# Kernel tuning notes

Hardware: AMD Instinct MI355X
Metric: run time of the kernel (lower is better)

Reference implementation:

```python
import jax, jax.numpy as jnp
import numpy as np

TEMPERATURE = 0.01
VMIN, VMAX = -1.0, 1.0
NUM_VALUES = 256


def setup_inputs() -> dict:
    key = jax.random.key(0)
    k_img, k_cmap = jax.random.split(key)
    image = jax.random.uniform(k_img, (4, 3, 512, 512), dtype=jnp.float32)
    cmap = jax.random.uniform(k_cmap, (NUM_VALUES, 3), dtype=jnp.float32)
    idx = jnp.arange(NUM_VALUES, dtype=jnp.float32)
    v_i = VMIN + (VMAX - VMIN) * idx / (NUM_VALUES - 1)
    return {"image": image, "cmap": cmap, "v_i": v_i}


def reference(image, cmap, v_i):
    # image: (N, 3, H, W) -> (N, H, W, 3)
    img = jnp.transpose(image, (0, 2, 3, 1))
    # squared euclidean distance to each of the 256 colormap colors
    # dist[n,h,w,k] = sum_c (img[n,h,w,c] - cmap[k,c])^2
    diff = img[..., None, :] - cmap  # (N, H, W, K, 3)
    distances = jnp.sum(diff * diff, axis=-1)  # (N, H, W, K)
    weights = jax.nn.softmax(-distances / TEMPERATURE, axis=-1)
    velocities = jnp.einsum('nhwk,k->nhw', weights, v_i)
    return velocities
```

## Files before the change

### kernel.cpp

```cpp
#include <hip/hip_runtime.h>


typedef float v2f __attribute__((ext_vector_type(2)));

#define HWSZ 262144
#define NPIX 1048576
#define K2F  144.2695040888963f

__global__ __launch_bounds__(256) void rgb2vel_prep(
    const float* __restrict__ cmap, const float* __restrict__ v_i,
    float4* __restrict__ ab, float* __restrict__ vv) {
  int k = threadIdx.x;
  float cx = cmap[k * 3 + 0];
  float cy = cmap[k * 3 + 1];
  float cz = cmap[k * 3 + 2];
  float4 r;
  r.x = 2.0f * K2F * cx;
  r.y = 2.0f * K2F * cy;
  r.z = 2.0f * K2F * cz;
  r.w = -K2F * (cx * cx + cy * cy + cz * cz);
  ab[k] = r;
  vv[k] = v_i[k];
}

__global__ __launch_bounds__(256) void rgb2vel_main(
    const float* __restrict__ img, const float4* __restrict__ ab,
    const float* __restrict__ vv, float* __restrict__ out) {
  int t = blockIdx.x * 256 + threadIdx.x;
  int n = t >> 17;
  int hw2 = (t & 131071) << 1;
  const float* base = img + (size_t)n * 3 * HWSZ + hw2;
  v2f px = {base[0], base[1]};
  v2f py = {base[HWSZ], base[HWSZ + 1]};
  v2f pz = {base[2 * HWSZ], base[2 * HWSZ + 1]};

  v2f mk2 = {-K2F, -K2F};
  v2f cp = __builtin_elementwise_fma(
               px, px, __builtin_elementwise_fma(py, py, pz * pz)) *
           mk2;

  v2f s = {0.0f, 0.0f};
  v2f sv = {0.0f, 0.0f};
#pragma unroll 16
  for (int k = 0; k < 256; ++k) {
    float4 c = ab[k];
    v2f cx = {c.x, c.x};
    v2f cy = {c.y, c.y};
    v2f cz = {c.z, c.z};
    v2f cw = {c.w, c.w};
    v2f a = __builtin_elementwise_fma(
        cx, px,
        __builtin_elementwise_fma(cy, py,
                                  __builtin_elementwise_fma(cz, pz, cw + cp)));
    v2f w;
    w.x = __builtin_amdgcn_exp2f(a.x);
    w.y = __builtin_amdgcn_exp2f(a.y);
    s = s + w;
    float vk = vv[k];
    v2f vkv = {vk, vk};
    sv = __builtin_elementwise_fma(w, vkv, sv);
  }
  float o0 = sv.x / s.x;
  float o1 = sv.y / s.y;
  size_t o = (size_t)2 * t;
  out[o] = o0;
  out[o + 1] = o1;
}

extern "C" void kernel_launch(void* const* d_in, const int* in_sizes, int n_in,
                              void* d_out, int out_size, void* d_ws, size_t ws_size,
                              hipStream_t stream) {
  const float* image = (const float*)d_in[0];
  const float* cmap  = (const float*)d_in[1];
  const float* v_i   = (const float*)d_in[2];
  float* out = (float*)d_out;

  float4* ab = (float4*)d_ws;
  float*  vv = (float*)((char*)d_ws + 256 * 16);

  rgb2vel_prep<<<1, 256, 0, stream>>>(cmap, v_i, ab, vv);
  rgb2vel_main<<<NPIX / 2 / 256, 256, 0, stream>>>(image, ab, vv, out);
}
```

Measured before the change: 103.2 us.

## Compute softmax logits with bf16 MFMA using split-precision operands

Moves the per-pixel, per-color dot product (logit computation) onto MFMA 16x16x32 bf16 instructions. Pixel and colormap values are split into hi/mid/lo bf16 components so the logits keep roughly fp32 accuracy. Partial sums are reduced through shared memory. The FMA work per pixel moves off the vector ALU and leaves mainly exp2 and accumulation there, at the cost of LDS traffic, added syncs and higher register pressure.

```diff
diff --git a/kernel.cpp b/kernel.cpp
--- a/kernel.cpp
+++ b/kernel.cpp
@@ -1,70 +1,150 @@
 #include <hip/hip_runtime.h>
 
 
-typedef float v2f __attribute__((ext_vector_type(2)));
+typedef __attribute__((ext_vector_type(8))) short short8;
+typedef __attribute__((ext_vector_type(4))) float f32x4;
 
 #define HWSZ 262144
 #define NPIX 1048576
 #define K2F  144.2695040888963f
 
-__global__ __launch_bounds__(256) void rgb2vel_prep(
-    const float* __restrict__ cmap, const float* __restrict__ v_i,
-    float4* __restrict__ ab, float* __restrict__ vv) {
-  int k = threadIdx.x;
-  float cx = cmap[k * 3 + 0];
-  float cy = cmap[k * 3 + 1];
-  float cz = cmap[k * 3 + 2];
-  float4 r;
-  r.x = 2.0f * K2F * cx;
-  r.y = 2.0f * K2F * cy;
-  r.z = 2.0f * K2F * cz;
-  r.w = -K2F * (cx * cx + cy * cy + cz * cz);
-  ab[k] = r;
-  vv[k] = v_i[k];
+static __device__ __forceinline__ unsigned f2bf(float x, float* resid) {
+  unsigned u = __builtin_bit_cast(unsigned, x);
+  unsigned r = (u + 0x7fffu + ((u >> 16) & 1u)) >> 16;
+  if (resid) *resid = x - __builtin_bit_cast(float, r << 16);
+  return r;
+}
+static __device__ __forceinline__ unsigned bfp(unsigned lo, unsigned hi) {
+  return (lo & 0xffffu) | (hi << 16);
 }
 
-__global__ __launch_bounds__(256) void rgb2vel_main(
-    const float* __restrict__ img, const float4* __restrict__ ab,
+__global__ __launch_bounds__(256) void rgb2vel_prep(
+    const float* __restrict__ cmap, float4* __restrict__ btab) {
+  int k = threadIdx.x;
+  float c0 = cmap[k * 3 + 0], c1 = cmap[k * 3 + 1], c2 = cmap[k * 3 + 2];
+  float cc[3] = {c0, c1, c2};
+  unsigned H[3], M[3], L[3];
+  float r;
+#pragma unroll
+  for (int ch = 0; ch < 3; ++ch) {
+    float x = 2.0f * K2F * cc[ch];
+    H[ch] = f2bf(x, &r);
+    M[ch] = f2bf(r, &r);
+    L[ch] = f2bf(r, nullptr);
+  }
+  float mcc = -(K2F * (c0 * c0 + c1 * c1 + c2 * c2));
+  unsigned mh = f2bf(mcc, &r);
+  unsigned mm = f2bf(r, &r);
+  unsigned ml = f2bf(r, nullptr);
+  const unsigned N1 = 0xBF80u;
+  unsigned d[16];
+  d[0] = bfp(H[0], H[1]); d[1] = bfp(H[2], H[0]); d[2] = bfp(H[1], H[2]);
+  d[3] = bfp(M[0], M[1]); d[4] = bfp(M[2], L[0]); d[5] = bfp(L[1], L[2]);
+  d[6] = bfp(M[0], M[1]); d[7] = bfp(M[2], H[0]); d[8] = bfp(H[1], H[2]);
+  d[9] = bfp(mh, mm);     d[10] = bfp(ml, N1);    d[11] = bfp(N1, N1);
+  d[12] = d[13] = d[14] = d[15] = 0u;
+  int col = k & 15, tt = k >> 4;
+#pragma unroll
+  for (int g = 0; g < 4; ++g) {
+    float4 v;
+    v.x = __builtin_bit_cast(float, d[4 * g + 0]);
+    v.y = __builtin_bit_cast(float, d[4 * g + 1]);
+    v.z = __builtin_bit_cast(float, d[4 * g + 2]);
+    v.w = __builtin_bit_cast(float, d[4 * g + 3]);
+    btab[tt * 64 + g * 16 + col] = v;
+  }
+}
+
+__global__ __launch_bounds__(256, 2) void rgb2vel_main(
+    const float* __restrict__ img, const float4* __restrict__ btab,
     const float* __restrict__ vv, float* __restrict__ out) {
-  int t = blockIdx.x * 256 + threadIdx.x;
-  int n = t >> 17;
-  int hw2 = (t & 131071) << 1;
-  const float* base = img + (size_t)n * 3 * HWSZ + hw2;
-  v2f px = {base[0], base[1]};
-  v2f py = {base[HWSZ], base[HWSZ + 1]};
-  v2f pz = {base[2 * HWSZ], base[2 * HWSZ + 1]};
+  __shared__ __align__(16) unsigned char smem[4 * 8704];
+  const int lane = threadIdx.x & 63;
+  const int warp = threadIdx.x >> 6;
+  unsigned char* wl = smem + warp * 8704;
+  const int wpix = blockIdx.x * 256 + warp * 64;
+  const int col = lane & 15;
+  const int g = lane >> 4;
 
-  v2f mk2 = {-K2F, -K2F};
-  v2f cp = __builtin_elementwise_fma(
-               px, px, __builtin_elementwise_fma(py, py, pz * pz)) *
-           mk2;
+  short8 bfr[16];
+  float vk[16];
+#pragma unroll
+  for (int t = 0; t < 16; ++t) {
+    bfr[t] = __builtin_bit_cast(short8, btab[t * 64 + lane]);
+    vk[t] = vv[t * 16 + col];
+  }
 
-  v2f s = {0.0f, 0.0f};
-  v2f sv = {0.0f, 0.0f};
-#pragma unroll 16
-  for (int k = 0; k < 256; ++k) {
-    float4 c = ab[k];
-    v2f cx = {c.x, c.x};
-    v2f cy = {c.y, c.y};
-    v2f cz = {c.z, c.z};
-    v2f cw = {c.w, c.w};
-    v2f a = __builtin_elementwise_fma(
-        cx, px,
-        __builtin_elementwise_fma(cy, py,
-                                  __builtin_elementwise_fma(cz, pz, cw + cp)));
-    v2f w;
-    w.x = __builtin_amdgcn_exp2f(a.x);
-    w.y = __builtin_amdgcn_exp2f(a.y);
-    s = s + w;
-    float vk = vv[k];
-    v2f vkv = {vk, vk};
-    sv = __builtin_elementwise_fma(w, vkv, sv);
+  {
+    int idx = wpix + lane;
+    int n = idx >> 18;
+    int hw = idx & (HWSZ - 1);
+    const float* pb = img + (size_t)n * 3 * HWSZ + hw;
+    float p0 = pb[0], p1 = pb[HWSZ], p2 = pb[2 * HWSZ];
+    float pc[3] = {p0, p1, p2};
+    unsigned ph[3], pm[3], pl[3];
+    float r;
+#pragma unroll
+    for (int ch = 0; ch < 3; ++ch) {
+      ph[ch] = f2bf(pc[ch], &r);
+      pm[ch] = f2bf(r, &r);
+      pl[ch] = f2bf(r, nullptr);
+    }
+    float q = K2F * (p0 * p0 + p1 * p1 + p2 * p2);
+    unsigned qh = f2bf(q, &r);
+    unsigned qm = f2bf(r, &r);
+    unsigned ql = f2bf(r, nullptr);
+    const unsigned ONE = 0x3F80u;
+    int4* sb = (int4*)(wl + lane * 80);
+    sb[0] = make_int4((int)bfp(ph[0], ph[1]), (int)bfp(ph[2], pm[0]),
+                      (int)bfp(pm[1], pm[2]), (int)bfp(ph[0], ph[1]));
+    sb[1] = make_int4((int)bfp(ph[2], ph[0]), (int)bfp(ph[1], ph[2]),
+                      (int)bfp(pm[0], pm[1]), (int)bfp(pm[2], pl[0]));
+    sb[2] = make_int4((int)bfp(pl[1], pl[2]), (int)bfp(ONE, ONE),
+                      (int)bfp(ONE, qh),      (int)bfp(qm, ql));
+    sb[3] = make_int4(0, 0, 0, 0);
   }
-  float o0 = sv.x / s.x;
-  float o1 = sv.y / s.y;
-  size_t o = (size_t)2 * t;
-  out[o] = o0;
-  out[o + 1] = o1;
+  __syncthreads();
+
+  short8 afr[4];
+#pragma unroll
+  for (int m = 0; m < 4; ++m)
+    afr[m] = *(const short8*)(wl + (m * 16 + col) * 80 + g * 16);
+
+  float s[16], sv[16];
+#pragma unroll
+  for (int i = 0; i < 16; ++i) { s[i] = 0.f; sv[i] = 0.f; }
+  const f32x4 z = {0.f, 0.f, 0.f, 0.f};
+
+#pragma unroll
+  for (int t = 0; t < 16; ++t) {
+#pragma unroll
+    for (int m = 0; m < 4; ++m) {
+      f32x4 c = __builtin_amdgcn_mfma_f32_16x16x32_bf16(afr[m], bfr[t], z, 0, 0, 0);
+#pragma unroll
+      for (int rr = 0; rr < 4; ++rr) {
+        float w = __builtin_amdgcn_exp2f(c[rr]);
+        s[m * 4 + rr] += w;
+        sv[m * 4 + rr] = fmaf(w, vk[t], sv[m * 4 + rr]);
+      }
+    }
+  }
+
+#pragma unroll
+  for (int m = 0; m < 4; ++m)
+#pragma unroll
+    for (int rr = 0; rr < 4; ++rr) {
+      int p = m * 16 + g * 4 + rr;
+      *(float2*)(wl + (p * 17 + col) * 8) = make_float2(s[m * 4 + rr], sv[m * 4 + rr]);
+    }
+  __syncthreads();
+  float st = 0.f, svt = 0.f;
+#pragma unroll
+  for (int c2 = 0; c2 < 16; ++c2) {
+    float2 v = *(const float2*)(wl + (lane * 17 + c2) * 8);
+    st += v.x;
+    svt += v.y;
+  }
+  out[wpix + lane] = svt / st;
 }
 
 extern "C" void kernel_launch(void* const* d_in, const int* in_sizes, int n_in,
@@ -75,9 +155,8 @@
   const float* v_i   = (const float*)d_in[2];
   float* out = (float*)d_out;
 
-  float4* ab = (float4*)d_ws;
-  float*  vv = (float*)((char*)d_ws + 256 * 16);
+  float4* btab = (float4*)d_ws;
 
-  rgb2vel_prep<<<1, 256, 0, stream>>>(cmap, v_i, ab, vv);
-  rgb2vel_main<<<NPIX / 2 / 256, 256, 0, stream>>>(image, ab, vv, out);
+  rgb2vel_prep<<<1, 256, 0, stream>>>(cmap, btab);
+  rgb2vel_main<<<NPIX / 256, 256, 0, stream>>>(image, btab, v_i, out);
 }
```

Result: faster. 99.28 us (-3.8%).
